# Performance work log

Hardware: AMD Instinct MI355X
Metric: run time of the kernel (lower is better)

Reference implementation:

```python
import jax, jax.numpy as jnp
import numpy as np

HIDDEN_DIM = 1024
NUM_HEADS = 8
CONTEXT_LEN = 8
HEAD_DIM = HIDDEN_DIM // NUM_HEADS


def setup_inputs() -> dict:
    key = jax.random.key(0)
    ks = jax.random.split(key, 6)
    B, C, H, W = 32, HIDDEN_DIM, 18, 32
    K = CONTEXT_LEN
    h_current = jax.random.normal(ks[0], (B, C, H, W), dtype=jnp.float32)
    h_buffer = jax.random.normal(ks[1], (K, B, C, H, W), dtype=jnp.float32)
    # Parameters (torch nn.Linear stores weight as [out, in]; y = x @ W.T + b)
    s_qkv = 1.0 / np.sqrt(C)
    W_qkv = jax.random.uniform(ks[2], (3 * C, C), jnp.float32, -s_qkv, s_qkv)
    W_out = jax.random.uniform(ks[3], (C, C), jnp.float32, -s_qkv, s_qkv)
    b_out = jax.random.uniform(ks[4], (C,), jnp.float32, -s_qkv, s_qkv)
    rel_emb = jax.random.normal(ks[5], (2 * CONTEXT_LEN + 1, NUM_HEADS), dtype=jnp.float32)
    return {"h_current": h_current, "h_buffer": h_buffer, "W_qkv": W_qkv,
            "W_out": W_out, "b_out": b_out, "rel_emb": rel_emb}


def reference(h_current, h_buffer, W_qkv, W_out, b_out, rel_emb):
    B, C, H, W = h_current.shape
    K = h_buffer.shape[0]
    T = K + 1
    nh, hd = NUM_HEADS, HEAD_DIM

    # spatial pooling (AdaptiveAvgPool2d(1)) then stack buffer frames + current
    pooled_buf = h_buffer.mean(axis=(3, 4))          # [K, B, C]
    pooled_cur = h_current.mean(axis=(2, 3))         # [B, C]
    context = jnp.concatenate(
        [jnp.transpose(pooled_buf, (1, 0, 2)), pooled_cur[:, None, :]], axis=1)  # [B, T, C]

    # QKV projection (no bias)
    qkv = context @ W_qkv.T                          # [B, T, 3C]
    q, k, v = jnp.split(qkv, 3, axis=-1)
    q = q.reshape(B, T, nh, hd).transpose(0, 2, 1, 3)  # [B, nh, T, hd]
    k = k.reshape(B, T, nh, hd).transpose(0, 2, 1, 3)
    v = v.reshape(B, T, nh, hd).transpose(0, 2, 1, 3)

    # relative-position bias
    idx = jnp.arange(T)
    rel = jnp.clip(idx[:, None] - idx[None, :], -CONTEXT_LEN, CONTEXT_LEN) + CONTEXT_LEN
    bias = rel_emb[rel]                              # [T, T, nh]
    bias = jnp.transpose(bias, (2, 0, 1))            # [nh, T, T]

    # causal mask (-inf above diagonal) combined with bias
    causal = jnp.triu(jnp.full((T, T), -jnp.inf, dtype=context.dtype), k=1)
    attn_mask = causal[None, None, :, :] + bias[None, :, :, :]  # [1, nh, T, T]

    scale = 1.0 / np.sqrt(hd)
    scores = jnp.einsum('bhqd,bhkd->bhqk', q, k) * scale + attn_mask
    attn = jax.nn.softmax(scores, axis=-1)
    attn_out = jnp.einsum('bhqk,bhkd->bhqd', attn, v)  # [B, nh, T, hd]
    attn_out = attn_out.transpose(0, 2, 1, 3).reshape(B, T, C)

    # output projection of final timestep, broadcast over spatial dims, residual
    out = attn_out[:, -1] @ W_out.T + b_out          # [B, C]
    return h_current + out[:, :, None, None]
```

## Files before the change

kernel.cpp:

```cpp
#include <hip/hip_runtime.h>
#include <hip/hip_bf16.h>

#define BB 32
#define CC 1024
#define HWSZ 576
#define KCTX 8
#define TT 9
#define NH 8
#define HD 128

#define NS 4
#define KV_MN (288 * 2048)
#define Q_MN  (32 * 1024)

typedef float v4f __attribute__((ext_vector_type(4)));
typedef __attribute__((ext_vector_type(8))) short  bf16x8;
typedef __attribute__((ext_vector_type(8))) ushort u16x8;
typedef __attribute__((ext_vector_type(4))) float  f32x4;

__device__ __forceinline__ ushort f2bf(float f) {
    uint u = __builtin_bit_cast(uint, f);
    return (ushort)((u + 0x7FFFu + ((u >> 16) & 1u)) >> 16);
}

__global__ __launch_bounds__(256) void pool_kernel(
    const float* __restrict__ hbuf,
    const float* __restrict__ hcur,
    const float* __restrict__ Wqkv,
    ushort* __restrict__ ctxb,
    ushort* __restrict__ Wb)
{
    const int wave = threadIdx.x >> 6;
    const int lane = threadIdx.x & 63;
    const int sub  = lane >> 4;
    const int l16  = lane & 15;
    const int stride = gridDim.x * 16;
    const int nrows = BB * TT * CC;

    for (int r0 = (blockIdx.x * 4 + wave) * 4; r0 < nrows; r0 += stride) {
        const int r = r0 + sub;
        v4f acc = {0.f, 0.f, 0.f, 0.f};
        int cidx;
        if (r < KCTX * BB * CC) {
            const v4f* s4 = (const v4f*)(hbuf + (size_t)r * HWSZ);
            const int t = r >> 15;
            const int b = (r >> 10) & 31;
            cidx = (b * TT + t) * CC + (r & (CC - 1));
#pragma unroll
            for (int j = 0; j < 9; ++j)
                acc += __builtin_nontemporal_load(s4 + l16 + 16 * j);
        } else {
            const int rc = r - KCTX * BB * CC;
            const v4f* s4 = (const v4f*)(hcur + (size_t)rc * HWSZ);
            cidx = ((rc >> 10) * TT + KCTX) * CC + (rc & (CC - 1));
#pragma unroll
            for (int j = 0; j < 9; ++j)
                acc += s4[l16 + 16 * j];
        }
        float sum = acc.x + acc.y + acc.z + acc.w;
        sum += __shfl_xor(sum, 1);
        sum += __shfl_xor(sum, 2);
        sum += __shfl_xor(sum, 4);
        sum += __shfl_xor(sum, 8);
        if (l16 == 0) ctxb[cidx] = f2bf(sum * (1.0f / 576.0f));
    }

    const int nchunk = 3072 * 1024 / 8;
    for (int idx = blockIdx.x * 256 + threadIdx.x; idx < nchunk;
         idx += gridDim.x * 256) {
        const float* src = Wqkv + (size_t)idx * 8;
        v4f a = *(const v4f*)src;
        v4f b = *(const v4f*)(src + 4);
        u16x8 o;
        o[0] = f2bf(a.x); o[1] = f2bf(a.y); o[2] = f2bf(a.z); o[3] = f2bf(a.w);
        o[4] = f2bf(b.x); o[5] = f2bf(b.y); o[6] = f2bf(b.z); o[7] = f2bf(b.w);
        *(u16x8*)(Wb + (size_t)idx * 8) = o;
    }
}

__global__ __launch_bounds__(256) void qkv_mfma(
    const ushort* __restrict__ ctxb, const ushort* __restrict__ Wb,
    float* __restrict__ qpart, float* __restrict__ kvpart)
{
    const int wave = threadIdx.x >> 6;
    const int lane = threadIdx.x & 63;
    const int t = blockIdx.x * 4 + wave;
    const int l15 = lane & 15;
    const int kg  = lane >> 4;

    const ushort* abase;
    const ushort* bbase;
    float* out;
    int ldy, outrow0, outcol0;

    if (t < 1152) {
        const int s  = t & 3;
        const int tt = t >> 2;
        const int mt = tt / 16, nt = tt % 16;
        const int k0 = s * 256;
        abase = ctxb + (size_t)(mt * 16 + l15) * 1024 + k0 + kg * 8;
        bbase = Wb + (size_t)(1024 + nt * 128 + l15) * 1024 + k0 + kg * 8;
        out = kvpart + (size_t)s * KV_MN;
        ldy = 2048;
        outrow0 = mt * 16 + kg * 4;
        outcol0 = nt * 128 + l15;
    } else {
        const int r  = t - 1152;
        const int s  = r & 3;
        const int tt = r >> 2;
        const int mt = tt >> 3, nt = tt & 7;
        const int k0 = s * 256;
        abase = ctxb + (size_t)((mt * 16 + l15) * 9 + 8) * 1024 + k0 + kg * 8;
        bbase = Wb + (size_t)(nt * 128 + l15) * 1024 + k0 + kg * 8;
        out = qpart + (size_t)s * Q_MN;
        ldy = 1024;
        outrow0 = mt * 16 + kg * 4;
        outcol0 = nt * 128 + l15;
    }

    f32x4 acc0 = {0,0,0,0}, acc1 = {0,0,0,0}, acc2 = {0,0,0,0}, acc3 = {0,0,0,0};
    f32x4 acc4 = {0,0,0,0}, acc5 = {0,0,0,0}, acc6 = {0,0,0,0}, acc7 = {0,0,0,0};

#pragma unroll
    for (int kk = 0; kk < 8; ++kk) {
        bf16x8 a = *(const bf16x8*)(abase + kk * 32);
        const ushort* bp = bbase + kk * 32;
        bf16x8 b0 = *(const bf16x8*)(bp + 0 * 16 * 1024);
        bf16x8 b1 = *(const bf16x8*)(bp + 1 * 16 * 1024);
        bf16x8 b2 = *(const bf16x8*)(bp + 2 * 16 * 1024);
        bf16x8 b3 = *(const bf16x8*)(bp + 3 * 16 * 1024);
        bf16x8 b4 = *(const bf16x8*)(bp + 4 * 16 * 1024);
        bf16x8 b5 = *(const bf16x8*)(bp + 5 * 16 * 1024);
        bf16x8 b6 = *(const bf16x8*)(bp + 6 * 16 * 1024);
        bf16x8 b7 = *(const bf16x8*)(bp + 7 * 16 * 1024);
        acc0 = __builtin_amdgcn_mfma_f32_16x16x32_bf16(a, b0, acc0, 0, 0, 0);
        acc1 = __builtin_amdgcn_mfma_f32_16x16x32_bf16(a, b1, acc1, 0, 0, 0);
        acc2 = __builtin_amdgcn_mfma_f32_16x16x32_bf16(a, b2, acc2, 0, 0, 0);
        acc3 = __builtin_amdgcn_mfma_f32_16x16x32_bf16(a, b3, acc3, 0, 0, 0);
        acc4 = __builtin_amdgcn_mfma_f32_16x16x32_bf16(a, b4, acc4, 0, 0, 0);
        acc5 = __builtin_amdgcn_mfma_f32_16x16x32_bf16(a, b5, acc5, 0, 0, 0);
        acc6 = __builtin_amdgcn_mfma_f32_16x16x32_bf16(a, b6, acc6, 0, 0, 0);
        acc7 = __builtin_amdgcn_mfma_f32_16x16x32_bf16(a, b7, acc7, 0, 0, 0);
    }

    float* yb = out + (size_t)outrow0 * ldy + outcol0;
#pragma unroll
    for (int i = 0; i < 4; ++i) {
        float* yr = yb + (size_t)i * ldy;
        yr[0 * 16] = acc0[i]; yr[1 * 16] = acc1[i];
        yr[2 * 16] = acc2[i]; yr[3 * 16] = acc3[i];
        yr[4 * 16] = acc4[i]; yr[5 * 16] = acc5[i];
        yr[6 * 16] = acc6[i]; yr[7 * 16] = acc7[i];
    }
}

__global__ __launch_bounds__(64) void attn_kernel(
    const float* __restrict__ kvpart,
    const float* __restrict__ qpart,
    const float* __restrict__ rel_emb,
    float* __restrict__ attn_out)
{
    const int lane = threadIdx.x;
    const int pair = blockIdx.x;
    const int b = pair >> 3;
    const int h = pair & 7;
    const float scale = 0.08838834764831845f;

    const int qoff = b * CC + h * HD;
    float q1 = 0.f, q2 = 0.f;
#pragma unroll
    for (int s = 0; s < NS; ++s) {
        q1 += qpart[(size_t)s * Q_MN + qoff + lane];
        q2 += qpart[(size_t)s * Q_MN + qoff + lane + 64];
    }
    q1 *= scale; q2 *= scale;

    float sc[TT];
#pragma unroll
    for (int j = 0; j < TT; ++j) {
        const size_t base = (size_t)(b * TT + j) * 2048 + h * HD;
        float k1 = 0.f, k2 = 0.f;
#pragma unroll
        for (int s = 0; s < NS; ++s) {
            k1 += kvpart[(size_t)s * KV_MN + base + lane];
            k2 += kvpart[(size_t)s * KV_MN + base + lane + 64];
        }
        float p = q1 * k1 + q2 * k2;
#pragma unroll
        for (int off = 32; off; off >>= 1) p += __shfl_xor(p, off);
        sc[j] = p + rel_emb[(2 * KCTX - j) * NH + h];
    }
    float m = sc[0];
#pragma unroll
    for (int j = 1; j < TT; ++j) m = fmaxf(m, sc[j]);
    float sum = 0.f;
#pragma unroll
    for (int j = 0; j < TT; ++j) { sc[j] = expf(sc[j] - m); sum += sc[j]; }
    const float inv = 1.0f / sum;

    float a1 = 0.f, a2 = 0.f;
#pragma unroll
    for (int j = 0; j < TT; ++j) {
        const size_t base = (size_t)(b * TT + j) * 2048 + 1024 + h * HD;
        float v1 = 0.f, v2 = 0.f;
#pragma unroll
        for (int s = 0; s < NS; ++s) {
            v1 += kvpart[(size_t)s * KV_MN + base + lane];
            v2 += kvpart[(size_t)s * KV_MN + base + lane + 64];
        }
        a1 += sc[j] * v1;
        a2 += sc[j] * v2;
    }
    attn_out[qoff + lane] = a1 * inv;
    attn_out[qoff + lane + 64] = a2 * inv;
}

__global__ __launch_bounds__(256) void final_fused(
    const float* __restrict__ hc,
    const float* __restrict__ attnb,
    const float* __restrict__ Wout,
    const float* __restrict__ bias,
    float* __restrict__ y)
{
    const int wave = threadIdx.x >> 6;
    const int lane = threadIdx.x & 63;
    const int stride = gridDim.x * 4;
    const int nrows = BB * CC;

    for (int r = blockIdx.x * 4 + wave; r < nrows; r += stride) {
        const int b = r >> 10;
        const int c = r & (CC - 1);

        const v4f* ar = (const v4f*)(attnb + (size_t)b * CC);
        const v4f* wr = (const v4f*)(Wout + (size_t)c * CC);
        v4f acc = {0.f, 0.f, 0.f, 0.f};
#pragma unroll
        for (int j = 0; j < 4; ++j) {
            v4f a = ar[lane + 64 * j];
            v4f w = wr[lane + 64 * j];
            acc += a * w;
        }
        float dot = acc.x + acc.y + acc.z + acc.w;
#pragma unroll
        for (int off = 32; off; off >>= 1) dot += __shfl_xor(dot, off);
        const float add = dot + bias[c];

        const v4f* s4 = (const v4f*)(hc + (size_t)r * HWSZ);
        v4f* d4 = (v4f*)(y + (size_t)r * HWSZ);
        v4f v0 = s4[lane];
        v0.x += add; v0.y += add; v0.z += add; v0.w += add;
        __builtin_nontemporal_store(v0, d4 + lane);
        v4f v1 = s4[lane + 64];
        v1.x += add; v1.y += add; v1.z += add; v1.w += add;
        __builtin_nontemporal_store(v1, d4 + lane + 64);
        if (lane < 16) {
            v4f v2 = s4[lane + 128];
            v2.x += add; v2.y += add; v2.z += add; v2.w += add;
            __builtin_nontemporal_store(v2, d4 + lane + 128);
        }
    }
}

extern "C" void kernel_launch(void* const* d_in, const int* in_sizes, int n_in,
                              void* d_out, int out_size, void* d_ws, size_t ws_size,
                              hipStream_t stream) {
    const float* h_current = (const float*)d_in[0];
    const float* h_buffer  = (const float*)d_in[1];
    const float* W_qkv     = (const float*)d_in[2];
    const float* W_out     = (const float*)d_in[3];
    const float* b_out     = (const float*)d_in[4];
    const float* rel_emb   = (const float*)d_in[5];

    ushort* ctxb = (ushort*)d_ws;
    ushort* Wb   = ctxb + 294912;
    float* kvpart = (float*)(Wb + 3145728);
    float* qpart  = kvpart + (size_t)NS * KV_MN;
    float* attnb  = qpart + (size_t)NS * Q_MN;

    pool_kernel<<<2048, 256, 0, stream>>>(h_buffer, h_current, W_qkv, ctxb, Wb);

    qkv_mfma<<<304, 256, 0, stream>>>(ctxb, Wb, qpart, kvpart);

    attn_kernel<<<BB * NH, 64, 0, stream>>>(kvpart, qpart, rel_emb, attnb);

    final_fused<<<2048, 256, 0, stream>>>(h_current, attnb, W_out, b_out, (float*)d_out);
}
```

Baseline: 154.6 us.

## Assign one output channel per block in final kernel to reuse W_out row

The final projection-plus-residual kernel now gives each block one output channel. All 32 batches compute their dot products against a single W_out row, which is reduced through shared memory, and the block then streams the 32 matching h_current rows. Before, each wave re-read a W_out row and an attention vector for every (b,c) row. The new layout cuts redundant W_out traffic, but the broadcast write now reads 32 strided row blocks per workgroup, the grid drops to 1024 blocks, and two barriers are added.

```diff
diff --git a/kernel.cpp b/kernel.cpp
--- a/kernel.cpp
+++ b/kernel.cpp
@@ -222,31 +222,38 @@
     const float* __restrict__ bias,
     float* __restrict__ y)
 {
-    const int wave = threadIdx.x >> 6;
-    const int lane = threadIdx.x & 63;
-    const int stride = gridDim.x * 4;
-    const int nrows = BB * CC;
-
-    for (int r = blockIdx.x * 4 + wave; r < nrows; r += stride) {
-        const int b = r >> 10;
-        const int c = r & (CC - 1);
-
-        const v4f* ar = (const v4f*)(attnb + (size_t)b * CC);
-        const v4f* wr = (const v4f*)(Wout + (size_t)c * CC);
-        v4f acc = {0.f, 0.f, 0.f, 0.f};
-#pragma unroll
-        for (int j = 0; j < 4; ++j) {
-            v4f a = ar[lane + 64 * j];
-            v4f w = wr[lane + 64 * j];
-            acc += a * w;
-        }
-        float dot = acc.x + acc.y + acc.z + acc.w;
-#pragma unroll
-        for (int off = 32; off; off >>= 1) dot += __shfl_xor(dot, off);
-        const float add = dot + bias[c];
-
-        const v4f* s4 = (const v4f*)(hc + (size_t)r * HWSZ);
-        v4f* d4 = (v4f*)(y + (size_t)r * HWSZ);
+    __shared__ float partial[256];
+    __shared__ float outs[BB];
+
+    const int c = blockIdx.x;
+    const int t = threadIdx.x;
+    const int b = t >> 3;
+    const int seg = t & 7;
+
+    const v4f* ar = (const v4f*)(attnb + (size_t)b * CC + seg * 128);
+    const v4f* wr = (const v4f*)(Wout + (size_t)c * CC + seg * 128);
+    v4f acc = {0.f, 0.f, 0.f, 0.f};
+#pragma unroll
+    for (int j = 0; j < 32; ++j) acc += ar[j] * wr[j];
+    partial[t] = acc.x + acc.y + acc.z + acc.w;
+    __syncthreads();
+    if (t < BB) {
+        float s = 0.f;
+#pragma unroll
+        for (int i = 0; i < 8; ++i) s += partial[t * 8 + i];
+        outs[t] = s + bias[c];
+    }
+    __syncthreads();
+
+    const int wave = t >> 6;
+    const int lane = t & 63;
+#pragma unroll
+    for (int i = 0; i < 8; ++i) {
+        const int bb = wave * 8 + i;
+        const float add = outs[bb];
+        const size_t r = (size_t)bb * CC + c;
+        const v4f* s4 = (const v4f*)(hc + r * HWSZ);
+        v4f* d4 = (v4f*)(y + r * HWSZ);
         v4f v0 = s4[lane];
         v0.x += add; v0.y += add; v0.z += add; v0.w += add;
         __builtin_nontemporal_store(v0, d4 + lane);
@@ -283,5 +290,5 @@
 
     attn_kernel<<<BB * NH, 64, 0, stream>>>(kvpart, qpart, rel_emb, attnb);
 
-    final_fused<<<2048, 256, 0, stream>>>(h_current, attnb, W_out, b_out, (float*)d_out);
-}
+    final_fused<<<CC, 256, 0, stream>>>(h_current, attnb, W_out, b_out, (float*)d_out);
+}
```

New measurement: 175.2 us. +13.3%, slower.
